# Kernel tuning notes

Measured on AMD Instinct MI355X. Metric: run time of the kernel, lower is better.

The kernel has to match this reference:

```python
import jax, jax.numpy as jnp
import numpy as np

NEG_SLOPE = 0.2

def _gatv2(x_src, x_dst, src, dst, Wl, bl, Wr, br, att, bias, num_dst, edge_feat=None, We=None):
    # PyG GATv2Conv (heads=1, add_self_loops=False, eval mode -> no dropout)
    xl = x_src @ Wl + bl                      # [Ns, C] lin_l on source
    xr = x_dst @ Wr + br                      # [Nd, C] lin_r on target
    m = xl[src] + xr[dst]                     # [E, C]
    if edge_feat is not None:
        m = m + edge_feat @ We                # lin_edge (bias=False)
    e = jax.nn.leaky_relu(m, NEG_SLOPE) @ att # [E] attention logits
    emax = jax.ops.segment_max(e, dst, num_segments=num_dst)
    ee = jnp.exp(e - emax[dst])
    denom = jax.ops.segment_sum(ee, dst, num_segments=num_dst)
    alpha = ee / jnp.maximum(denom[dst], 1e-16)
    out = jax.ops.segment_sum(alpha[:, None] * xl[src], dst, num_segments=num_dst)
    return out + bias


def setup_inputs() -> dict:
    key = jax.random.key(0)
    N_OP, N_M, N_A = 50000, 5000, 2000
    C_OP, C_M, C_A = 256, 128, 128
    E_OO, E_OM, E_MA, E_DIM = 200000, 200000, 60000, 8
    ks = jax.random.split(key, 40)
    i = iter(range(40))
    def nrm(shape, fan_in):
        return jax.random.normal(ks[next(i)], shape, dtype=jnp.float32) / np.sqrt(fan_in)
    inp = {}
    inp['x_op'] = jax.random.normal(ks[next(i)], (N_OP, C_OP), dtype=jnp.float32)
    inp['x_m'] = jax.random.normal(ks[next(i)], (N_M, C_M), dtype=jnp.float32)
    inp['x_a'] = jax.random.normal(ks[next(i)], (N_A, C_A), dtype=jnp.float32)
    inp['ei_pred'] = jax.random.randint(ks[next(i)], (2, E_OO), 0, N_OP)
    inp['ei_succ'] = jax.random.randint(ks[next(i)], (2, E_OO), 0, N_OP)
    inp['src_o2m'] = jax.random.randint(ks[next(i)], (E_OM,), 0, N_OP)
    inp['dst_o2m'] = jax.random.randint(ks[next(i)], (E_OM,), 0, N_M)
    inp['src_m2a'] = jax.random.randint(ks[next(i)], (E_MA,), 0, N_M)
    inp['dst_m2a'] = jax.random.randint(ks[next(i)], (E_MA,), 0, N_A)
    inp['ea_m2a'] = jax.random.normal(ks[next(i)], (E_MA, E_DIM), dtype=jnp.float32)
    for name, c_in_src, c_in_dst, c_out in [('pred', C_OP, C_OP, C_OP), ('succ', C_OP, C_OP, C_OP), ('o2m', C_OP, C_M, C_M), ('m2a', C_M, C_A, C_A)]:
        inp[f'Wl_{name}'] = nrm((c_in_src, c_out), c_in_src)
        inp[f'bl_{name}'] = jnp.zeros((c_out,), jnp.float32)
        inp[f'Wr_{name}'] = nrm((c_in_dst, c_out), c_in_dst)
        inp[f'br_{name}'] = jnp.zeros((c_out,), jnp.float32)
        inp[f'att_{name}'] = nrm((c_out,), c_out)
        inp[f'b_{name}'] = jnp.zeros((c_out,), jnp.float32)
    inp['We_m2a'] = nrm((E_DIM, C_A), E_DIM)
    return inp


def reference(x_op, x_m, x_a, ei_pred, ei_succ, src_o2m, dst_o2m, src_m2a, dst_m2a, ea_m2a,
              Wl_pred, bl_pred, Wr_pred, br_pred, att_pred, b_pred,
              Wl_succ, bl_succ, Wr_succ, br_succ, att_succ, b_succ,
              Wl_o2m, bl_o2m, Wr_o2m, br_o2m, att_o2m, b_o2m,
              Wl_m2a, bl_m2a, Wr_m2a, br_m2a, att_m2a, b_m2a, We_m2a):
    N_OP, N_M, N_A = x_op.shape[0], x_m.shape[0], x_a.shape[0]
    # operation_relation_extract: two op->op GATv2 convs, HeteroConv sum-aggregated
    f_pred = _gatv2(x_op, x_op, ei_pred[0], ei_pred[1], Wl_pred, bl_pred, Wr_pred, br_pred, att_pred, b_pred, N_OP)
    f_succ = _gatv2(x_op, x_op, ei_succ[0], ei_succ[1], Wl_succ, bl_succ, Wr_succ, br_succ, att_succ, b_succ, N_OP)
    # hetero_relation_extract
    f_mach = _gatv2(x_op, x_m, src_o2m, dst_o2m, Wl_o2m, bl_o2m, Wr_o2m, br_o2m, att_o2m, b_o2m, N_M)
    f_agv = _gatv2(x_m, x_a, src_m2a, dst_m2a, Wl_m2a, bl_m2a, Wr_m2a, br_m2a, att_m2a, b_m2a, N_A, edge_feat=ea_m2a, We=We_m2a)
    # residual sum across relation outputs per node type
    out_op = x_op + f_pred + f_succ
    out_m = x_m + f_mach
    out_a = x_a + f_agv
    return (out_op, out_m, out_a)
```

## Files before the change

kernel.cpp:

```cpp
#include <hip/hip_runtime.h>

#define N_OP   50000
#define N_M    5000
#define N_A    2000
#define C_OP   256
#define C_M    128
#define C_A    128
#define E_OO   200000
#define E_OM   200000
#define E_MA   60000
#define E_DIM  8

#define OUT_OP_OFF 0
#define OUT_M_OFF  (N_OP * C_OP)
#define OUT_A_OFF  (N_OP * C_OP + N_M * C_M)

typedef short bf16x8 __attribute__((ext_vector_type(8)));
typedef float f32x4 __attribute__((ext_vector_type(4)));
typedef __attribute__((address_space(1))) const unsigned gu32;
typedef __attribute__((address_space(3))) unsigned lu32;

__device__ __forceinline__ unsigned short f2bf(float f) {
    unsigned u = __float_as_uint(f);
    unsigned r = (u + 0x7FFFu + ((u >> 16) & 1u)) >> 16;
    return (unsigned short)r;
}
__device__ __forceinline__ float bf2f(unsigned short h) {
    return __uint_as_float(((unsigned)h) << 16);
}

__device__ __forceinline__ void init_one(const float* __restrict__ x,
                                         const float* __restrict__ b1,
                                         const float* __restrict__ b2,
                                         float* __restrict__ out,
                                         unsigned short* __restrict__ xc,
                                         int i, int cmask) {
    float4 v = ((const float4*)x)[i];
    const int cb = i & cmask;
    float4 b = ((const float4*)b1)[cb];
    if (b2) {
        float4 t = ((const float4*)b2)[cb];
        b.x += t.x; b.y += t.y; b.z += t.z; b.w += t.w;
    }
    float4 o;
    o.x = v.x + b.x; o.y = v.y + b.y; o.z = v.z + b.z; o.w = v.w + b.w;
    ((float4*)out)[i] = o;
    ushort4 r;
    r.x = f2bf(v.x); r.y = f2bf(v.y); r.z = f2bf(v.z); r.w = f2bf(v.w);
    ((ushort4*)xc)[i] = r;
}

#define I3_OP (N_OP * C_OP / 4)
#define I3_M  (I3_OP + N_M * C_M / 4)
#define I3_A  (I3_M + N_A * C_A / 4)

__global__ void init3(const float* __restrict__ x_op, const float* __restrict__ x_m,
                      const float* __restrict__ x_a,
                      const float* __restrict__ bP, const float* __restrict__ bS,
                      const float* __restrict__ bO, const float* __restrict__ bA,
                      float* __restrict__ out_op, float* __restrict__ out_m,
                      float* __restrict__ out_a,
                      unsigned short* __restrict__ xcop, unsigned short* __restrict__ xcm,
                      unsigned short* __restrict__ xca) {
    int i = blockIdx.x * blockDim.x + threadIdx.x;
    if (i < I3_OP)      init_one(x_op, bP, bS, out_op, xcop, i, 63);
    else if (i < I3_M)  init_one(x_m, bO, nullptr, out_m, xcm, i - I3_OP, 31);
    else if (i < I3_A)  init_one(x_a, bA, nullptr, out_a, xca, i - I3_M, 31);
}

#define PK_P   131072
#define PK_S   262144
#define PK_OL  294912
#define PK_OR  311296
#define PK_ML  327680
#define PK_MR  344064
#define PK_BP  344576
#define PK_BS  345088

__global__ void pack_all(const float* __restrict__ WlP, const float* __restrict__ WrP,
                         const float* __restrict__ WlS, const float* __restrict__ WrS,
                         const float* __restrict__ WOl, const float* __restrict__ WOr,
                         const float* __restrict__ WMl, const float* __restrict__ WMr,
                         const float* __restrict__ blP, const float* __restrict__ brP,
                         const float* __restrict__ blS, const float* __restrict__ brS,
                         unsigned short* __restrict__ BtP, unsigned short* __restrict__ BtS,
                         unsigned short* __restrict__ BtOL, unsigned short* __restrict__ BtOR,
                         unsigned short* __restrict__ BtML, unsigned short* __restrict__ BtMR,
                         float* __restrict__ biasP, float* __restrict__ biasS) {
    int i = blockIdx.x * blockDim.x + threadIdx.x;
    if (i < PK_P) {
        int n = i >> 8, k = i & 255;
        BtP[i] = f2bf((n < 256) ? WlP[k * 256 + n] : WrP[k * 256 + (n - 256)]);
    } else if (i < PK_S) {
        int j = i - PK_P; int n = j >> 8, k = j & 255;
        BtS[j] = f2bf((n < 256) ? WlS[k * 256 + n] : WrS[k * 256 + (n - 256)]);
    } else if (i < PK_OL) {
        int j = i - PK_S; int n = j >> 8, k = j & 255;
        BtOL[j] = f2bf(WOl[k * 128 + n]);
    } else if (i < PK_OR) {
        int j = i - PK_OL; int n = j >> 7, k = j & 127;
        BtOR[j] = f2bf(WOr[k * 128 + n]);
    } else if (i < PK_ML) {
        int j = i - PK_OR; int n = j >> 7, k = j & 127;
        BtML[j] = f2bf(WMl[k * 128 + n]);
    } else if (i < PK_MR) {
        int j = i - PK_ML; int n = j >> 7, k = j & 127;
        BtMR[j] = f2bf(WMr[k * 128 + n]);
    } else if (i < PK_BP) {
        int j = i - PK_MR;
        biasP[j] = (j < 256) ? blP[j] : brP[j - 256];
    } else if (i < PK_BS) {
        int j = i - PK_BP;
        biasS[j] = (j < 256) ? blS[j] : brS[j - 256];
    }
}

__device__ __forceinline__ void gload_lds16(const void* g, void* l) {
    __builtin_amdgcn_global_load_lds((gu32*)g, (lu32*)l, 16, 0, 0);
}

__global__ __launch_bounds__(256) void mfma_gemm(
    const unsigned short* __restrict__ A, const unsigned short* __restrict__ Bt,
    const float* __restrict__ bias, unsigned short* __restrict__ C,
    int M, int K, int ldc) {
    __shared__ unsigned short As[2][128 * 64];
    __shared__ unsigned short Bs[2][128 * 64];

    const int tid  = threadIdx.x;
    const int lane = tid & 63;
    const int wid  = tid >> 6;
    const int m0   = blockIdx.x * 128;
    const int n0   = blockIdx.y * 128;

    f32x4 acc[4][4] = {};

    const int srow   = tid >> 3;
    const int scolb  = (tid & 7) * 16;
    const int scole  = (scolb ^ ((srow & 7) << 4)) >> 1;

    int grA[4], grB[4];
#pragma unroll
    for (int i = 0; i < 4; ++i) {
        int gr = m0 + i * 32 + srow;
        grA[i] = (gr < M) ? gr : M - 1;
        grB[i] = n0 + i * 32 + srow;
    }

    const int nt = K >> 6;
    int cur = 0;

#define STAGE(buf, k0)                                                          \
    {                                                                           \
        _Pragma("unroll")                                                       \
        for (int i = 0; i < 4; ++i)                                             \
            gload_lds16(A + (size_t)grA[i] * K + (k0) + scole,                  \
                        &As[buf][i * 2048 + tid * 8]);                          \
        _Pragma("unroll")                                                       \
        for (int i = 0; i < 4; ++i)                                             \
            gload_lds16(Bt + (size_t)grB[i] * K + (k0) + scole,                 \
                        &Bs[buf][i * 2048 + tid * 8]);                          \
    }

    STAGE(0, 0)
    asm volatile("s_waitcnt vmcnt(0)" ::: "memory");
    __syncthreads();

    const int wr = (wid >> 1) * 64;
    const int wc = (wid & 1) * 64;

    for (int t = 0; t < nt; ++t) {
        if (t + 1 < nt) STAGE(cur ^ 1, (t + 1) * 64)
#pragma unroll
        for (int kh = 0; kh < 2; ++kh) {
            const int kob = kh * 64 + (lane >> 4) * 16;
            bf16x8 a[4], b[4];
#pragma unroll
            for (int mi = 0; mi < 4; ++mi) {
                const int row = wr + mi * 16 + (lane & 15);
                a[mi] = *(const bf16x8*)((const char*)As[cur] + row * 128 +
                                         (kob ^ ((row & 7) << 4)));
            }
#pragma unroll
            for (int ni = 0; ni < 4; ++ni) {
                const int row = wc + ni * 16 + (lane & 15);
                b[ni] = *(const bf16x8*)((const char*)Bs[cur] + row * 128 +
                                         (kob ^ ((row & 7) << 4)));
            }
#pragma unroll
            for (int mi = 0; mi < 4; ++mi)
#pragma unroll
                for (int ni = 0; ni < 4; ++ni)
                    acc[mi][ni] = __builtin_amdgcn_mfma_f32_16x16x32_bf16(
                        a[mi], b[ni], acc[mi][ni], 0, 0, 0);
        }
        asm volatile("s_waitcnt vmcnt(0)" ::: "memory");
        __syncthreads();
        cur ^= 1;
    }
#undef STAGE

    const int crow = (lane >> 4) * 4;
    const int ccol = lane & 15;
    float bcol[4];
#pragma unroll
    for (int ni = 0; ni < 4; ++ni) bcol[ni] = bias[n0 + wc + ni * 16 + ccol];
#pragma unroll
    for (int mi = 0; mi < 4; ++mi) {
#pragma unroll
        for (int j = 0; j < 4; ++j) {
            const int row = m0 + wr + mi * 16 + crow + j;
            if (row < M) {
                unsigned short* pc = C + (size_t)row * ldc + n0 + wc + ccol;
#pragma unroll
                for (int ni = 0; ni < 4; ++ni)
                    pc[ni * 16] = f2bf(acc[mi][ni][j] + bcol[ni]);
            }
        }
    }
}

template <int K, int N, int TM>
__global__ void gemm_ef(const float* __restrict__ A, const float* __restrict__ W,
                        const int* __restrict__ eid, unsigned short* __restrict__ out) {
    __shared__ float As[TM][K];
    const int m0 = blockIdx.x * TM;
    const int tid = threadIdx.x;
    for (int idx = tid; idx < TM * K; idx += N) {
        int r = idx / K, k = idx - r * K;
        As[r][k] = A[(size_t)eid[m0 + r] * K + k];
    }
    __syncthreads();
    float acc[TM] = {};
    for (int k = 0; k < K; ++k) {
        const float w = W[k * N + tid];
#pragma unroll
        for (int r = 0; r < TM; ++r) acc[r] += As[r][k] * w;
    }
#pragma unroll
    for (int r = 0; r < TM; ++r) out[(size_t)(m0 + r) * N + tid] = f2bf(acc[r]);
}

#define NB_P 49
#define NB_S 49
#define NB_O 5
#define NB_A 2
#define NTOT 107000
#define ETOT 660000

__global__ void zero4(int* __restrict__ p, int n) {
    int i = blockIdx.x * blockDim.x + threadIdx.x;
    if (i < n) p[i] = 0;
}

__global__ void hist_rank4(const int* __restrict__ dP, const int* __restrict__ dS,
                           const int* __restrict__ dO, const int* __restrict__ dA,
                           int* __restrict__ cP, int* __restrict__ cS,
                           int* __restrict__ cO, int* __restrict__ cA,
                           int* __restrict__ rk) {
    int i = blockIdx.x * blockDim.x + threadIdx.x;
    if (i < 200000)      rk[i] = atomicAdd(&cP[dP[i]], 1);
    else if (i < 400000) rk[i] = atomicAdd(&cS[dS[i - 200000]], 1);
    else if (i < 600000) rk[i] = atomicAdd(&cO[dO[i - 400000]], 1);
    else if (i < ETOT)   rk[i] = atomicAdd(&cA[dA[i - 600000]], 1);
}

__global__ void scan_blk4(const int* __restrict__ cP, const int* __restrict__ cS,
                          const int* __restrict__ cO, const int* __restrict__ cA,
                          int* __restrict__ pP, int* __restrict__ pS,
                          int* __restrict__ pO, int* __restrict__ pA,
                          int* __restrict__ bsum) {
    __shared__ int smem[1024];
    int b = blockIdx.x;
    const int* cnt; int* ptr; int n; int bo;
    if (b < NB_P)                { cnt = cP; ptr = pP; n = 50000; bo = 0; }
    else if (b < NB_P + NB_S)    { cnt = cS; ptr = pS; n = 50000; bo = 64;  b -= NB_P; }
    else if (b < NB_P + NB_S + NB_O) { cnt = cO; ptr = pO; n = 5000; bo = 128; b -= NB_P + NB_S; }
    else                         { cnt = cA; ptr = pA; n = 2000; bo = 192; b -= NB_P + NB_S + NB_O; }
    const int tid = threadIdx.x;
    const int i = b * 1024 + tid;
    const int v = (i < n) ? cnt[i] : 0;
    smem[tid] = v;
    __syncthreads();
    for (int o = 1; o < 1024; o <<= 1) {
        int t = (tid >= o) ? smem[tid - o] : 0;
        __syncthreads();
        smem[tid] += t;
        __syncthreads();
    }
    if (i < n) ptr[i] = smem[tid] - v;
    if (tid == 1023) bsum[bo + b] = smem[1023];
}

__global__ void scan_tops4(const int* __restrict__ bsum, int* __restrict__ boff,
                           int* __restrict__ pP, int* __restrict__ pS,
                           int* __restrict__ pO, int* __restrict__ pA) {
    __shared__ int smem[1024];
    const int seg = blockIdx.x;
    const int nb = (seg < 2) ? 49 : (seg == 2 ? 5 : 2);
    const int off = seg * 64;
    int* ptr_n = (seg == 0) ? pP + 50000 : (seg == 1) ? pS + 50000
               : (seg == 2) ? pO + 5000 : pA + 2000;
    const int tid = threadIdx.x;
    const int v = (tid < nb) ? bsum[off + tid] : 0;
    smem[tid] = v;
    __syncthreads();
    for (int o = 1; o < 1024; o <<= 1) {
        int t = (tid >= o) ? smem[tid - o] : 0;
        __syncthreads();
        smem[tid] += t;
        __syncthreads();
    }
    if (tid < nb) boff[off + tid] = smem[tid] - v;
    if (tid == 1023) *ptr_n = smem[1023];
}

__global__ void scan_add4(int* __restrict__ pP, int* __restrict__ pS,
                          int* __restrict__ pO, int* __restrict__ pA,
                          const int* __restrict__ boff) {
    int i = blockIdx.x * blockDim.x + threadIdx.x;
    int* ptr; int loc; int off;
    if (i < 50000)       { ptr = pP; loc = i;          off = 0; }
    else if (i < 100000) { ptr = pS; loc = i - 50000;  off = 64; }
    else if (i < 105000) { ptr = pO; loc = i - 100000; off = 128; }
    else if (i < NTOT)   { ptr = pA; loc = i - 105000; off = 192; }
    else return;
    ptr[loc] += boff[off + (loc >> 10)];
}

__global__ void scatter_nr4(const int* __restrict__ sP, const int* __restrict__ dP,
                            const int* __restrict__ sS, const int* __restrict__ dS,
                            const int* __restrict__ sO, const int* __restrict__ dO,
                            const int* __restrict__ sA, const int* __restrict__ dA,
                            const int* __restrict__ pP, const int* __restrict__ pS,
                            const int* __restrict__ pO, const int* __restrict__ pA,
                            const int* __restrict__ rk,
                            int* __restrict__ srP, int* __restrict__ srS,
                            int* __restrict__ srO, int* __restrict__ srA,
                            int* __restrict__ eiA) {
    int i = blockIdx.x * blockDim.x + threadIdx.x;
    if (i < 200000) {
        srP[pP[dP[i]] + rk[i]] = sP[i];
    } else if (i < 400000) {
        const int j = i - 200000;
        srS[pS[dS[j]] + rk[i]] = sS[j];
    } else if (i < 600000) {
        const int j = i - 400000;
        srO[pO[dO[j]] + rk[i]] = sO[j];
    } else if (i < ETOT) {
        const int j = i - 600000;
        const int pos = pA[dA[j]] + rk[i];
        srA[pos] = sA[j];
        eiA[pos] = j;
    }
}

template <int C>
__global__ void csr_serial2(const unsigned short* __restrict__ xl, int ldl,
                            const unsigned short* __restrict__ xr, int ldr,
                            const float* __restrict__ att,
                            const int* __restrict__ ptr, const int* __restrict__ srcs,
                            float* __restrict__ out, int n) {
    const int tid = threadIdx.x;
    const int node = blockIdx.x * (blockDim.x >> 5) + (tid >> 5);
    if (node >= n) return;
    const int gl = tid & 31;
    const int beg = ptr[node], end = ptr[node + 1];
    if (beg == end) return;

    constexpr int V = C / 32;
    const int c0 = gl * V;

    float av[V], rvf[V];
    {
        const unsigned short* pr = xr + (size_t)node * ldr + c0;
        unsigned short rv[V];
        *(uint4*)rv = *(const uint4*)pr;
#pragma unroll
        for (int v4 = 0; v4 < V / 4; ++v4)
            *(float4*)(av + v4 * 4) = ((const float4*)(att + c0))[v4];
#pragma unroll
        for (int v = 0; v < V; ++v) rvf[v] = bf2f(rv[v]);
    }

    float runM = -3.0e38f, runS = 0.0f;
    float acc[V] = {};

    unsigned short lv[V];
    {
        const unsigned short* pl = xl + (size_t)srcs[beg] * ldl + c0;
        *(uint4*)lv = *(const uint4*)pl;
    }

    for (int j = beg; j < end; ++j) {
        float cf[V];
#pragma unroll
        for (int v = 0; v < V; ++v) cf[v] = bf2f(lv[v]);
        if (j + 1 < end) {
            const unsigned short* pl = xl + (size_t)srcs[j + 1] * ldl + c0;
            *(uint4*)lv = *(const uint4*)pl;
        }

        float part = 0.0f;
#pragma unroll
        for (int v = 0; v < V; ++v) {
            float m = cf[v] + rvf[v];
            m = (m >= 0.0f) ? m : 0.2f * m;
            part += m * av[v];
        }
        part += __shfl_xor(part, 1, 64);
        part += __shfl_xor(part, 2, 64);
        part += __shfl_xor(part, 4, 64);
        part += __shfl_xor(part, 8, 64);
        part += __shfl_xor(part, 16, 64);

        const float newM = fmaxf(runM, part);
        const float sc = __expf(runM - newM);
        const float e1 = __expf(part - newM);
        runS = runS * sc + e1;
        runM = newM;
#pragma unroll
        for (int v = 0; v < V; ++v) acc[v] = acc[v] * sc + e1 * cf[v];
    }

    const float inv = 1.0f / fmaxf(runS, 1e-16f);
    float* po = out + (size_t)node * C + c0;
#pragma unroll
    for (int v4 = 0; v4 < V / 4; ++v4) {
        float4 o = ((float4*)po)[v4];
        o.x += acc[v4 * 4 + 0] * inv;
        o.y += acc[v4 * 4 + 1] * inv;
        o.z += acc[v4 * 4 + 2] * inv;
        o.w += acc[v4 * 4 + 3] * inv;
        ((float4*)po)[v4] = o;
    }
}

template <int C, bool HAS_EF>
__global__ void csr_grp(const unsigned short* __restrict__ xl, int ldl,
                        const unsigned short* __restrict__ xr, int ldr,
                        const unsigned short* __restrict__ ef,
                        const float* __restrict__ att,
                        const int* __restrict__ ptr, const int* __restrict__ srcs,
                        float* __restrict__ out, int n) {
    const int node = blockIdx.x * (blockDim.x >> 6) + (threadIdx.x >> 6);
    if (node >= n) return;
    const int lane = threadIdx.x & 63;
    const int grp  = lane >> 4;
    const int sl   = lane & 15;
    const int beg = ptr[node], end = ptr[node + 1];
    if (beg == end) return;

    constexpr int W = C / 16;
    const int c0 = sl * W;

    float av[W], rvf[W];
    {
        const unsigned short* pr = xr + (size_t)node * ldr + c0;
        unsigned short rv[W];
        *(uint4*)rv = *(const uint4*)pr;
        if constexpr (W == 16) *(uint4*)(rv + 8) = *(const uint4*)(pr + 8);
#pragma unroll
        for (int v4 = 0; v4 < W / 4; ++v4)
            *(float4*)(av + v4 * 4) = ((const float4*)(att + c0))[v4];
#pragma unroll
        for (int v = 0; v < W; ++v) rvf[v] = bf2f(rv[v]);
    }

    float runM = -3.0e38f, runS = 0.0f;
    float acc[W] = {};

    for (int cb = beg; cb < end; cb += 4) {
        const int j = cb + grp;
        const bool act = (j < end);
        const int js = act ? j : end - 1;
        const int s = srcs[js];

        const unsigned short* pl = xl + (size_t)s * ldl + c0;
        unsigned short lv[W];
        *(uint4*)lv = *(const uint4*)pl;
        if constexpr (W == 16) *(uint4*)(lv + 8) = *(const uint4*)(pl + 8);
        float cf[W];
#pragma unroll
        for (int v = 0; v < W; ++v) cf[v] = bf2f(lv[v]);

        float part = 0.0f;
        if constexpr (HAS_EF) {
            unsigned short efv[W];
            const unsigned short* pe = ef + (size_t)js * C + c0;
            *(uint4*)efv = *(const uint4*)pe;
            if constexpr (W == 16) *(uint4*)(efv + 8) = *(const uint4*)(pe + 8);
#pragma unroll
            for (int v = 0; v < W; ++v) {
                float m = cf[v] + rvf[v] + bf2f(efv[v]);
                m = (m >= 0.0f) ? m : 0.2f * m;
                part += m * av[v];
            }
        } else {
#pragma unroll
            for (int v = 0; v < W; ++v) {
                float m = cf[v] + rvf[v];
                m = (m >= 0.0f) ? m : 0.2f * m;
                part += m * av[v];
            }
        }
        part += __shfl_xor(part, 1, 64);
        part += __shfl_xor(part, 2, 64);
        part += __shfl_xor(part, 4, 64);
        part += __shfl_xor(part, 8, 64);
        if (!act) part = -3.0e38f;

        float cm = fmaxf(part, __shfl_xor(part, 16, 64));
        cm = fmaxf(cm, __shfl_xor(cm, 32, 64));

        if (cm > runM) {
            const float sc = __expf(runM - cm);
            runS *= sc;
#pragma unroll
            for (int v = 0; v < W; ++v) acc[v] *= sc;
            runM = cm;
        }
        const float w = act ? __expf(part - runM) : 0.0f;
        float cs = w + __shfl_xor(w, 16, 64);
        cs += __shfl_xor(cs, 32, 64);
        runS += cs;
#pragma unroll
        for (int v = 0; v < W; ++v) acc[v] += w * cf[v];
    }

#pragma unroll
    for (int v = 0; v < W; ++v) acc[v] += __shfl_xor(acc[v], 16, 64);
#pragma unroll
    for (int v = 0; v < W; ++v) acc[v] += __shfl_xor(acc[v], 32, 64);

    const float inv = 1.0f / fmaxf(runS, 1e-16f);
    if (grp == 0) {
        float* po = out + (size_t)node * C + c0;
#pragma unroll
        for (int v4 = 0; v4 < W / 4; ++v4) {
            float4 o = ((float4*)po)[v4];
            o.x += acc[v4 * 4 + 0] * inv;
            o.y += acc[v4 * 4 + 1] * inv;
            o.z += acc[v4 * 4 + 2] * inv;
            o.w += acc[v4 * 4 + 3] * inv;
            ((float4*)po)[v4] = o;
        }
    }
}

#define F_H      0
#define F_XCOP   12800000
#define F_XCM    19200000
#define F_XCA    19520000
#define F_BTP    19648000
#define F_BTS    19713536
#define F_BTOL   19779072
#define F_BTOR   19795456
#define F_BTML   19803648
#define F_BTMR   19811840
#define F_BIASP  19820032
#define F_BIASS  19820544
#define F_CNT4   19821056
#define F_BSUM   19928056
#define F_BOFF   19928312
#define F_PTR_P  19928568
#define F_SRC_P  19978569
#define F_PTR_S  20178569
#define F_SRC_S  20228570
#define F_PTR_O  20428570
#define F_SRC_O  20433571
#define F_PTR_A  20633571
#define F_SRC_A  20635572
#define F_EID_A  20695572
#define F_RANK   20755572

extern "C" void kernel_launch(void* const* d_in, const int* in_sizes, int n_in,
                              void* d_out, int out_size, void* d_ws, size_t ws_size,
                              hipStream_t stream) {
    const float* x_op    = (const float*)d_in[0];
    const float* x_m     = (const float*)d_in[1];
    const float* x_a     = (const float*)d_in[2];
    const int*   ei_pred = (const int*)d_in[3];
    const int*   ei_succ = (const int*)d_in[4];
    const int*   src_o2m = (const int*)d_in[5];
    const int*   dst_o2m = (const int*)d_in[6];
    const int*   src_m2a = (const int*)d_in[7];
    const int*   dst_m2a = (const int*)d_in[8];
    const float* ea_m2a  = (const float*)d_in[9];

    const float* Wl_pred = (const float*)d_in[10];
    const float* bl_pred = (const float*)d_in[11];
    const float* Wr_pred = (const float*)d_in[12];
    const float* br_pred = (const float*)d_in[13];
    const float* att_pred= (const float*)d_in[14];
    const float* b_pred  = (const float*)d_in[15];

    const float* Wl_succ = (const float*)d_in[16];
    const float* bl_succ = (const float*)d_in[17];
    const float* Wr_succ = (const float*)d_in[18];
    const float* br_succ = (const float*)d_in[19];
    const float* att_succ= (const float*)d_in[20];
    const float* b_succ  = (const float*)d_in[21];

    const float* Wl_o2m  = (const float*)d_in[22];
    const float* bl_o2m  = (const float*)d_in[23];
    const float* Wr_o2m  = (const float*)d_in[24];
    const float* br_o2m  = (const float*)d_in[25];
    const float* att_o2m = (const float*)d_in[26];
    const float* b_o2m   = (const float*)d_in[27];

    const float* Wl_m2a  = (const float*)d_in[28];
    const float* bl_m2a  = (const float*)d_in[29];
    const float* Wr_m2a  = (const float*)d_in[30];
    const float* br_m2a  = (const float*)d_in[31];
    const float* att_m2a = (const float*)d_in[32];
    const float* b_m2a   = (const float*)d_in[33];
    const float* We_m2a  = (const float*)d_in[34];

    float* ws = (float*)d_ws;
    unsigned short* H     = (unsigned short*)(ws + F_H);
    unsigned short* xc_op = (unsigned short*)(ws + F_XCOP);
    unsigned short* xc_m  = (unsigned short*)(ws + F_XCM);
    unsigned short* xc_a  = (unsigned short*)(ws + F_XCA);
    unsigned short* BtP   = (unsigned short*)(ws + F_BTP);
    unsigned short* BtS   = (unsigned short*)(ws + F_BTS);
    unsigned short* BtOL  = (unsigned short*)(ws + F_BTOL);
    unsigned short* BtOR  = (unsigned short*)(ws + F_BTOR);
    unsigned short* BtML  = (unsigned short*)(ws + F_BTML);
    unsigned short* BtMR  = (unsigned short*)(ws + F_BTMR);
    float* biasP = ws + F_BIASP;
    float* biasS = ws + F_BIASS;
    int* cntP = (int*)(ws + F_CNT4);
    int* cntS = cntP + 50000;
    int* cntO = cntP + 100000;
    int* cntA = cntP + 105000;
    int* bsum = (int*)(ws + F_BSUM);
    int* boff = (int*)(ws + F_BOFF);
    int* ptrP = (int*)(ws + F_PTR_P); int* srcP = (int*)(ws + F_SRC_P);
    int* ptrS = (int*)(ws + F_PTR_S); int* srcS = (int*)(ws + F_SRC_S);
    int* ptrO = (int*)(ws + F_PTR_O); int* srcO = (int*)(ws + F_SRC_O);
    int* ptrA = (int*)(ws + F_PTR_A); int* srcA = (int*)(ws + F_SRC_A);
    int* eidA = (int*)(ws + F_EID_A);
    int* rk   = (int*)(ws + F_RANK);

    float* out_op = (float*)d_out + OUT_OP_OFF;
    float* out_m  = (float*)d_out + OUT_M_OFF;
    float* out_a  = (float*)d_out + OUT_A_OFF;

    zero4<<<(NTOT + 255) / 256, 256, 0, stream>>>(cntP, NTOT);
    hist_rank4<<<(ETOT + 255) / 256, 256, 0, stream>>>(ei_pred + E_OO, ei_succ + E_OO,
                                                       dst_o2m, dst_m2a,
                                                       cntP, cntS, cntO, cntA, rk);
    scan_blk4<<<NB_P + NB_S + NB_O + NB_A, 1024, 0, stream>>>(cntP, cntS, cntO, cntA,
                                                              ptrP, ptrS, ptrO, ptrA, bsum);
    scan_tops4<<<4, 1024, 0, stream>>>(bsum, boff, ptrP, ptrS, ptrO, ptrA);
    scan_add4<<<(NTOT + 255) / 256, 256, 0, stream>>>(ptrP, ptrS, ptrO, ptrA, boff);
    scatter_nr4<<<(ETOT + 255) / 256, 256, 0, stream>>>(
        ei_pred, ei_pred + E_OO, ei_succ, ei_succ + E_OO,
        src_o2m, dst_o2m, src_m2a, dst_m2a,
        ptrP, ptrS, ptrO, ptrA, rk,
        srcP, srcS, srcO, srcA, eidA);

    init3<<<(I3_A + 255) / 256, 256, 0, stream>>>(x_op, x_m, x_a, b_pred, b_succ, b_o2m, b_m2a,
                                                  out_op, out_m, out_a, xc_op, xc_m, xc_a);
    pack_all<<<(PK_BS + 255) / 256, 256, 0, stream>>>(
        Wl_pred, Wr_pred, Wl_succ, Wr_succ, Wl_o2m, Wr_o2m, Wl_m2a, Wr_m2a,
        bl_pred, br_pred, bl_succ, br_succ,
        BtP, BtS, BtOL, BtOR, BtML, BtMR, biasP, biasS);

    const int MT_OP = (N_OP + 127) / 128;
    const int MT_M  = (N_M + 127) / 128;
    const int MT_A  = (N_A + 127) / 128;

    mfma_gemm<<<dim3(MT_OP, 4), 256, 0, stream>>>(xc_op, BtP, biasP, H, N_OP, 256, 512);
    csr_serial2<256><<<(N_OP + 7) / 8, 256, 0, stream>>>(H, 512, H + 256, 512,
                                                         att_pred, ptrP, srcP, out_op, N_OP);

    mfma_gemm<<<dim3(MT_OP, 4), 256, 0, stream>>>(xc_op, BtS, biasS, H, N_OP, 256, 512);
    csr_serial2<256><<<(N_OP + 7) / 8, 256, 0, stream>>>(H, 512, H + 256, 512,
                                                         att_succ, ptrS, srcS, out_op, N_OP);

    {
        unsigned short* xlb = H;
        unsigned short* xrb = H + 6400000;
        mfma_gemm<<<dim3(MT_OP, 1), 256, 0, stream>>>(xc_op, BtOL, bl_o2m, xlb, N_OP, 256, 128);
        mfma_gemm<<<dim3(MT_M, 1), 256, 0, stream>>>(xc_m, BtOR, br_o2m, xrb, N_M, 128, 128);
        csr_grp<128, false><<<(N_M + 3) / 4, 256, 0, stream>>>(xlb, 128, xrb, 128, nullptr,
                                                               att_o2m, ptrO, srcO, out_m, N_M);
    }

    {
        unsigned short* xlb = H;
        unsigned short* xrb = H + 1000000;
        unsigned short* efb = H + 2000000;
        mfma_gemm<<<dim3(MT_M, 1), 256, 0, stream>>>(xc_m, BtML, bl_m2a, xlb, N_M, 128, 128);
        mfma_gemm<<<dim3(MT_A, 1), 256, 0, stream>>>(xc_a, BtMR, br_m2a, xrb, N_A, 128, 128);
        gemm_ef<8, 128, 4><<<E_MA / 4, 128, 0, stream>>>(ea_m2a, We_m2a, eidA, efb);
        csr_grp<128, true><<<(N_A + 3) / 4, 256, 0, stream>>>(xlb, 128, xrb, 128, efb,
                                                              att_m2a, ptrA, srcA, out_a, N_A);
    }
}
```

Before: 308.7 us.

## Merge independent prep, scatter, and small GEMM launches into combined kernels

Folds histogram/rank, input init/bf16 conversion, and weight packing into one prep_all kernel. The CSR scatter now runs as extra blocks of the first pred GEMM launch. The o2m lin_l/lin_r GEMMs become one gemm_pair launch, and the m2a GEMMs plus the edge-feature projection become one gemm_tri launch. The aim is fewer launches and idle gaps between small kernels. In exchange, the scatter blocks allocate GEMM-sized shared memory, which may lower their occupancy.

```diff
diff --git a/kernel.cpp b/kernel.cpp
--- a/kernel.cpp
+++ b/kernel.cpp
@@ -28,6 +28,27 @@
 __device__ __forceinline__ float bf2f(unsigned short h) {
     return __uint_as_float(((unsigned)h) << 16);
 }
+
+#define NTOT 107000
+#define ETOT 660000
+
+#define I3_OP (N_OP * C_OP / 4)
+#define I3_M  (I3_OP + N_M * C_M / 4)
+#define I3_A  (I3_M + N_A * C_A / 4)
+
+#define PK_P   131072
+#define PK_S   262144
+#define PK_OL  294912
+#define PK_OR  311296
+#define PK_ML  327680
+#define PK_MR  344064
+#define PK_BP  344576
+#define PK_BS  345088
+
+#define PREP_HIST_BLK ((ETOT + 255) / 256)
+#define PREP_INIT_BLK (I3_A / 256)
+#define PREP_PACK_BLK (PK_BS / 256)
+#define PREP_TOTAL    (PREP_HIST_BLK + PREP_INIT_BLK + PREP_PACK_BLK)
 
 __device__ __forceinline__ void init_one(const float* __restrict__ x,
                                          const float* __restrict__ b1,
@@ -50,68 +71,68 @@
     ((ushort4*)xc)[i] = r;
 }
 
-#define I3_OP (N_OP * C_OP / 4)
-#define I3_M  (I3_OP + N_M * C_M / 4)
-#define I3_A  (I3_M + N_A * C_A / 4)
-
-__global__ void init3(const float* __restrict__ x_op, const float* __restrict__ x_m,
-                      const float* __restrict__ x_a,
-                      const float* __restrict__ bP, const float* __restrict__ bS,
-                      const float* __restrict__ bO, const float* __restrict__ bA,
-                      float* __restrict__ out_op, float* __restrict__ out_m,
-                      float* __restrict__ out_a,
-                      unsigned short* __restrict__ xcop, unsigned short* __restrict__ xcm,
-                      unsigned short* __restrict__ xca) {
-    int i = blockIdx.x * blockDim.x + threadIdx.x;
-    if (i < I3_OP)      init_one(x_op, bP, bS, out_op, xcop, i, 63);
-    else if (i < I3_M)  init_one(x_m, bO, nullptr, out_m, xcm, i - I3_OP, 31);
-    else if (i < I3_A)  init_one(x_a, bA, nullptr, out_a, xca, i - I3_M, 31);
-}
-
-#define PK_P   131072
-#define PK_S   262144
-#define PK_OL  294912
-#define PK_OR  311296
-#define PK_ML  327680
-#define PK_MR  344064
-#define PK_BP  344576
-#define PK_BS  345088
-
-__global__ void pack_all(const float* __restrict__ WlP, const float* __restrict__ WrP,
-                         const float* __restrict__ WlS, const float* __restrict__ WrS,
-                         const float* __restrict__ WOl, const float* __restrict__ WOr,
-                         const float* __restrict__ WMl, const float* __restrict__ WMr,
-                         const float* __restrict__ blP, const float* __restrict__ brP,
-                         const float* __restrict__ blS, const float* __restrict__ brS,
-                         unsigned short* __restrict__ BtP, unsigned short* __restrict__ BtS,
-                         unsigned short* __restrict__ BtOL, unsigned short* __restrict__ BtOR,
-                         unsigned short* __restrict__ BtML, unsigned short* __restrict__ BtMR,
-                         float* __restrict__ biasP, float* __restrict__ biasS) {
-    int i = blockIdx.x * blockDim.x + threadIdx.x;
-    if (i < PK_P) {
-        int n = i >> 8, k = i & 255;
-        BtP[i] = f2bf((n < 256) ? WlP[k * 256 + n] : WrP[k * 256 + (n - 256)]);
-    } else if (i < PK_S) {
-        int j = i - PK_P; int n = j >> 8, k = j & 255;
-        BtS[j] = f2bf((n < 256) ? WlS[k * 256 + n] : WrS[k * 256 + (n - 256)]);
-    } else if (i < PK_OL) {
-        int j = i - PK_S; int n = j >> 8, k = j & 255;
-        BtOL[j] = f2bf(WOl[k * 128 + n]);
-    } else if (i < PK_OR) {
-        int j = i - PK_OL; int n = j >> 7, k = j & 127;
-        BtOR[j] = f2bf(WOr[k * 128 + n]);
-    } else if (i < PK_ML) {
-        int j = i - PK_OR; int n = j >> 7, k = j & 127;
-        BtML[j] = f2bf(WMl[k * 128 + n]);
-    } else if (i < PK_MR) {
-        int j = i - PK_ML; int n = j >> 7, k = j & 127;
-        BtMR[j] = f2bf(WMr[k * 128 + n]);
-    } else if (i < PK_BP) {
-        int j = i - PK_MR;
-        biasP[j] = (j < 256) ? blP[j] : brP[j - 256];
-    } else if (i < PK_BS) {
-        int j = i - PK_BP;
-        biasS[j] = (j < 256) ? blS[j] : brS[j - 256];
+__global__ void prep_all(
+    const int* __restrict__ dP, const int* __restrict__ dS,
+    const int* __restrict__ dO, const int* __restrict__ dA,
+    int* __restrict__ cP, int* __restrict__ cS,
+    int* __restrict__ cO, int* __restrict__ cA, int* __restrict__ rk,
+    const float* __restrict__ x_op, const float* __restrict__ x_m,
+    const float* __restrict__ x_a,
+    const float* __restrict__ bP, const float* __restrict__ bS,
+    const float* __restrict__ bO, const float* __restrict__ bA,
+    float* __restrict__ out_op, float* __restrict__ out_m, float* __restrict__ out_a,
+    unsigned short* __restrict__ xcop, unsigned short* __restrict__ xcm,
+    unsigned short* __restrict__ xca,
+    const float* __restrict__ WlP, const float* __restrict__ WrP,
+    const float* __restrict__ WlS, const float* __restrict__ WrS,
+    const float* __restrict__ WOl, const float* __restrict__ WOr,
+    const float* __restrict__ WMl, const float* __restrict__ WMr,
+    const float* __restrict__ blP, const float* __restrict__ brP,
+    const float* __restrict__ blS, const float* __restrict__ brS,
+    unsigned short* __restrict__ BtP, unsigned short* __restrict__ BtS,
+    unsigned short* __restrict__ BtOL, unsigned short* __restrict__ BtOR,
+    unsigned short* __restrict__ BtML, unsigned short* __restrict__ BtMR,
+    float* __restrict__ biasP, float* __restrict__ biasS) {
+    const int b = blockIdx.x;
+    const int tid = threadIdx.x;
+    if (b < PREP_HIST_BLK) {
+        int i = b * 256 + tid;
+        if (i < 200000)      rk[i] = atomicAdd(&cP[dP[i]], 1);
+        else if (i < 400000) rk[i] = atomicAdd(&cS[dS[i - 200000]], 1);
+        else if (i < 600000) rk[i] = atomicAdd(&cO[dO[i - 400000]], 1);
+        else if (i < ETOT)   rk[i] = atomicAdd(&cA[dA[i - 600000]], 1);
+    } else if (b < PREP_HIST_BLK + PREP_INIT_BLK) {
+        int i = (b - PREP_HIST_BLK) * 256 + tid;
+        if (i < I3_OP)      init_one(x_op, bP, bS, out_op, xcop, i, 63);
+        else if (i < I3_M)  init_one(x_m, bO, nullptr, out_m, xcm, i - I3_OP, 31);
+        else                init_one(x_a, bA, nullptr, out_a, xca, i - I3_M, 31);
+    } else {
+        int i = (b - PREP_HIST_BLK - PREP_INIT_BLK) * 256 + tid;
+        if (i < PK_P) {
+            int n = i >> 8, k = i & 255;
+            BtP[i] = f2bf((n < 256) ? WlP[k * 256 + n] : WrP[k * 256 + (n - 256)]);
+        } else if (i < PK_S) {
+            int j = i - PK_P; int n = j >> 8, k = j & 255;
+            BtS[j] = f2bf((n < 256) ? WlS[k * 256 + n] : WrS[k * 256 + (n - 256)]);
+        } else if (i < PK_OL) {
+            int j = i - PK_S; int n = j >> 8, k = j & 255;
+            BtOL[j] = f2bf(WOl[k * 128 + n]);
+        } else if (i < PK_OR) {
+            int j = i - PK_OL; int n = j >> 7, k = j & 127;
+            BtOR[j] = f2bf(WOr[k * 128 + n]);
+        } else if (i < PK_ML) {
+            int j = i - PK_OR; int n = j >> 7, k = j & 127;
+            BtML[j] = f2bf(WMl[k * 128 + n]);
+        } else if (i < PK_MR) {
+            int j = i - PK_ML; int n = j >> 7, k = j & 127;
+            BtMR[j] = f2bf(WMr[k * 128 + n]);
+        } else if (i < PK_BP) {
+            int j = i - PK_MR;
+            biasP[j] = (j < 256) ? blP[j] : brP[j - 256];
+        } else if (i < PK_BS) {
+            int j = i - PK_BP;
+            biasS[j] = (j < 256) ? blS[j] : brS[j - 256];
+        }
     }
 }
 
@@ -119,18 +140,16 @@
     __builtin_amdgcn_global_load_lds((gu32*)g, (lu32*)l, 16, 0, 0);
 }
 
-__global__ __launch_bounds__(256) void mfma_gemm(
+__device__ __forceinline__ void gemm_body(
     const unsigned short* __restrict__ A, const unsigned short* __restrict__ Bt,
     const float* __restrict__ bias, unsigned short* __restrict__ C,
-    int M, int K, int ldc) {
-    __shared__ unsigned short As[2][128 * 64];
-    __shared__ unsigned short Bs[2][128 * 64];
-
+    int M, int K, int ldc, int bx, int by,
+    unsigned short (&As)[2][128 * 64], unsigned short (&Bs)[2][128 * 64]) {
     const int tid  = threadIdx.x;
     const int lane = tid & 63;
     const int wid  = tid >> 6;
-    const int m0   = blockIdx.x * 128;
-    const int n0   = blockIdx.y * 128;
+    const int m0   = bx * 128;
+    const int n0   = by * 128;
 
     f32x4 acc[4][4] = {};
 
@@ -219,49 +238,113 @@
     }
 }
 
-template <int K, int N, int TM>
-__global__ void gemm_ef(const float* __restrict__ A, const float* __restrict__ W,
-                        const int* __restrict__ eid, unsigned short* __restrict__ out) {
-    __shared__ float As[TM][K];
-    const int m0 = blockIdx.x * TM;
-    const int tid = threadIdx.x;
-    for (int idx = tid; idx < TM * K; idx += N) {
-        int r = idx / K, k = idx - r * K;
-        As[r][k] = A[(size_t)eid[m0 + r] * K + k];
-    }
-    __syncthreads();
-    float acc[TM] = {};
-    for (int k = 0; k < K; ++k) {
-        const float w = W[k * N + tid];
-#pragma unroll
-        for (int r = 0; r < TM; ++r) acc[r] += As[r][k] * w;
-    }
-#pragma unroll
-    for (int r = 0; r < TM; ++r) out[(size_t)(m0 + r) * N + tid] = f2bf(acc[r]);
+__global__ __launch_bounds__(256) void mfma_gemm(
+    const unsigned short* __restrict__ A, const unsigned short* __restrict__ Bt,
+    const float* __restrict__ bias, unsigned short* __restrict__ C,
+    int M, int K, int ldc) {
+    __shared__ unsigned short As[2][128 * 64];
+    __shared__ unsigned short Bs[2][128 * 64];
+    gemm_body(A, Bt, bias, C, M, K, ldc, blockIdx.x, blockIdx.y, As, Bs);
+}
+
+#define SCAT_XBLK 645
+__global__ __launch_bounds__(256) void gemm_scat(
+    const unsigned short* __restrict__ A, const unsigned short* __restrict__ Bt,
+    const float* __restrict__ bias, unsigned short* __restrict__ C,
+    int M, int K, int ldc, int mt,
+    const int* __restrict__ sP, const int* __restrict__ dP,
+    const int* __restrict__ sS, const int* __restrict__ dS,
+    const int* __restrict__ sO, const int* __restrict__ dO,
+    const int* __restrict__ sA, const int* __restrict__ dA,
+    const int* __restrict__ pP, const int* __restrict__ pS,
+    const int* __restrict__ pO, const int* __restrict__ pA,
+    const int* __restrict__ rk,
+    int* __restrict__ srP, int* __restrict__ srS,
+    int* __restrict__ srO, int* __restrict__ srA, int* __restrict__ eiA) {
+    __shared__ unsigned short As[2][128 * 64];
+    __shared__ unsigned short Bs[2][128 * 64];
+    if ((int)blockIdx.x < mt) {
+        gemm_body(A, Bt, bias, C, M, K, ldc, blockIdx.x, blockIdx.y, As, Bs);
+    } else {
+        const int i = (((int)blockIdx.x - mt) * 4 + (int)blockIdx.y) * 256 + (int)threadIdx.x;
+        if (i < 200000) {
+            srP[pP[dP[i]] + rk[i]] = sP[i];
+        } else if (i < 400000) {
+            const int j = i - 200000;
+            srS[pS[dS[j]] + rk[i]] = sS[j];
+        } else if (i < 600000) {
+            const int j = i - 400000;
+            srO[pO[dO[j]] + rk[i]] = sO[j];
+        } else if (i < ETOT) {
+            const int j = i - 600000;
+            const int pos = pA[dA[j]] + rk[i];
+            srA[pos] = sA[j];
+            eiA[pos] = j;
+        }
+    }
+}
+
+__global__ __launch_bounds__(256) void gemm_pair(
+    const unsigned short* A1, const unsigned short* Bt1, const float* b1,
+    unsigned short* C1, int M1, int K1, int l1, int n1,
+    const unsigned short* A2, const unsigned short* Bt2, const float* b2,
+    unsigned short* C2, int M2, int K2, int l2) {
+    __shared__ unsigned short As[2][128 * 64];
+    __shared__ unsigned short Bs[2][128 * 64];
+    const unsigned short *A, *Bt; const float* bi; unsigned short* C;
+    int M, K, ldc, bx;
+    if ((int)blockIdx.x < n1) { A = A1; Bt = Bt1; bi = b1; C = C1; M = M1; K = K1; ldc = l1; bx = blockIdx.x; }
+    else                      { A = A2; Bt = Bt2; bi = b2; C = C2; M = M2; K = K2; ldc = l2; bx = blockIdx.x - n1; }
+    gemm_body(A, Bt, bi, C, M, K, ldc, bx, blockIdx.y, As, Bs);
+}
+
+__global__ __launch_bounds__(256) void gemm_tri(
+    const unsigned short* A1, const unsigned short* Bt1, const float* b1,
+    unsigned short* C1, int M1, int K1, int n1,
+    const unsigned short* A2, const unsigned short* Bt2, const float* b2,
+    unsigned short* C2, int M2, int K2, int n12,
+    const float* __restrict__ ea, const float* __restrict__ We,
+    const int* __restrict__ eid, unsigned short* __restrict__ efo) {
+    __shared__ unsigned short As[2][128 * 64];
+    __shared__ unsigned short Bs[2][128 * 64];
+    __shared__ float Ef[8][8];
+    const int b = blockIdx.x;
+    if (b < n12) {
+        const unsigned short *A, *Bt; const float* bi; unsigned short* C;
+        int M, K, bx;
+        if (b < n1) { A = A1; Bt = Bt1; bi = b1; C = C1; M = M1; K = K1; bx = b; }
+        else        { A = A2; Bt = Bt2; bi = b2; C = C2; M = M2; K = K2; bx = b - n1; }
+        gemm_body(A, Bt, bi, C, M, K, 128, bx, 0, As, Bs);
+    } else {
+        const int eb = b - n12;
+        const int m0 = eb * 8;
+        const int tid = threadIdx.x;
+        if (tid < 64) {
+            int r = tid >> 3, k = tid & 7;
+            Ef[r][k] = ea[(size_t)eid[m0 + r] * 8 + k];
+        }
+        __syncthreads();
+        const int col = tid & 127, half = tid >> 7;
+        float acc[4] = {};
+        for (int k = 0; k < 8; ++k) {
+            const float w = We[k * 128 + col];
+#pragma unroll
+            for (int r = 0; r < 4; ++r) acc[r] += Ef[half * 4 + r][k] * w;
+        }
+#pragma unroll
+        for (int r = 0; r < 4; ++r)
+            efo[(size_t)(m0 + half * 4 + r) * 128 + col] = f2bf(acc[r]);
+    }
 }
 
 #define NB_P 49
 #define NB_S 49
 #define NB_O 5
 #define NB_A 2
-#define NTOT 107000
-#define ETOT 660000
 
 __global__ void zero4(int* __restrict__ p, int n) {
     int i = blockIdx.x * blockDim.x + threadIdx.x;
     if (i < n) p[i] = 0;
-}
-
-__global__ void hist_rank4(const int* __restrict__ dP, const int* __restrict__ dS,
-                           const int* __restrict__ dO, const int* __restrict__ dA,
-                           int* __restrict__ cP, int* __restrict__ cS,
-                           int* __restrict__ cO, int* __restrict__ cA,
-                           int* __restrict__ rk) {
-    int i = blockIdx.x * blockDim.x + threadIdx.x;
-    if (i < 200000)      rk[i] = atomicAdd(&cP[dP[i]], 1);
-    else if (i < 400000) rk[i] = atomicAdd(&cS[dS[i - 200000]], 1);
-    else if (i < 600000) rk[i] = atomicAdd(&cO[dO[i - 400000]], 1);
-    else if (i < ETOT)   rk[i] = atomicAdd(&cA[dA[i - 600000]], 1);
 }
 
 __global__ void scan_blk4(const int* __restrict__ cP, const int* __restrict__ cS,
@@ -325,33 +408,6 @@
     else if (i < NTOT)   { ptr = pA; loc = i - 105000; off = 192; }
     else return;
     ptr[loc] += boff[off + (loc >> 10)];
-}
-
-__global__ void scatter_nr4(const int* __restrict__ sP, const int* __restrict__ dP,
-                            const int* __restrict__ sS, const int* __restrict__ dS,
-                            const int* __restrict__ sO, const int* __restrict__ dO,
-                            const int* __restrict__ sA, const int* __restrict__ dA,
-                            const int* __restrict__ pP, const int* __restrict__ pS,
-                            const int* __restrict__ pO, const int* __restrict__ pA,
-                            const int* __restrict__ rk,
-                            int* __restrict__ srP, int* __restrict__ srS,
-                            int* __restrict__ srO, int* __restrict__ srA,
-                            int* __restrict__ eiA) {
-    int i = blockIdx.x * blockDim.x + threadIdx.x;
-    if (i < 200000) {
-        srP[pP[dP[i]] + rk[i]] = sP[i];
-    } else if (i < 400000) {
-        const int j = i - 200000;
-        srS[pS[dS[j]] + rk[i]] = sS[j];
-    } else if (i < 600000) {
-        const int j = i - 400000;
-        srO[pO[dO[j]] + rk[i]] = sO[j];
-    } else if (i < ETOT) {
-        const int j = i - 600000;
-        const int pos = pA[dA[j]] + rk[i];
-        srA[pos] = sA[j];
-        eiA[pos] = j;
-    }
 }
 
 template <int C>
@@ -647,31 +703,31 @@
     float* out_a  = (float*)d_out + OUT_A_OFF;
 
     zero4<<<(NTOT + 255) / 256, 256, 0, stream>>>(cntP, NTOT);
-    hist_rank4<<<(ETOT + 255) / 256, 256, 0, stream>>>(ei_pred + E_OO, ei_succ + E_OO,
-                                                       dst_o2m, dst_m2a,
-                                                       cntP, cntS, cntO, cntA, rk);
+
+    prep_all<<<PREP_TOTAL, 256, 0, stream>>>(
+        ei_pred + E_OO, ei_succ + E_OO, dst_o2m, dst_m2a,
+        cntP, cntS, cntO, cntA, rk,
+        x_op, x_m, x_a, b_pred, b_succ, b_o2m, b_m2a,
+        out_op, out_m, out_a, xc_op, xc_m, xc_a,
+        Wl_pred, Wr_pred, Wl_succ, Wr_succ, Wl_o2m, Wr_o2m, Wl_m2a, Wr_m2a,
+        bl_pred, br_pred, bl_succ, br_succ,
+        BtP, BtS, BtOL, BtOR, BtML, BtMR, biasP, biasS);
+
     scan_blk4<<<NB_P + NB_S + NB_O + NB_A, 1024, 0, stream>>>(cntP, cntS, cntO, cntA,
                                                               ptrP, ptrS, ptrO, ptrA, bsum);
     scan_tops4<<<4, 1024, 0, stream>>>(bsum, boff, ptrP, ptrS, ptrO, ptrA);
     scan_add4<<<(NTOT + 255) / 256, 256, 0, stream>>>(ptrP, ptrS, ptrO, ptrA, boff);
-    scatter_nr4<<<(ETOT + 255) / 256, 256, 0, stream>>>(
+
+    const int MT_OP = (N_OP + 127) / 128;
+    const int MT_M  = (N_M + 127) / 128;
+    const int MT_A  = (N_A + 127) / 128;
+
+    gemm_scat<<<dim3(MT_OP + SCAT_XBLK, 4), 256, 0, stream>>>(
+        xc_op, BtP, biasP, H, N_OP, 256, 512, MT_OP,
         ei_pred, ei_pred + E_OO, ei_succ, ei_succ + E_OO,
         src_o2m, dst_o2m, src_m2a, dst_m2a,
         ptrP, ptrS, ptrO, ptrA, rk,
         srcP, srcS, srcO, srcA, eidA);
-
-    init3<<<(I3_A + 255) / 256, 256, 0, stream>>>(x_op, x_m, x_a, b_pred, b_succ, b_o2m, b_m2a,
-                                                  out_op, out_m, out_a, xc_op, xc_m, xc_a);
-    pack_all<<<(PK_BS + 255) / 256, 256, 0, stream>>>(
-        Wl_pred, Wr_pred, Wl_succ, Wr_succ, Wl_o2m, Wr_o2m, Wl_m2a, Wr_m2a,
-        bl_pred, br_pred, bl_succ, br_succ,
-        BtP, BtS, BtOL, BtOR, BtML, BtMR, biasP, biasS);
-
-    const int MT_OP = (N_OP + 127) / 128;
-    const int MT_M  = (N_M + 127) / 128;
-    const int MT_A  = (N_A + 127) / 128;
-
-    mfma_gemm<<<dim3(MT_OP, 4), 256, 0, stream>>>(xc_op, BtP, biasP, H, N_OP, 256, 512);
     csr_serial2<256><<<(N_OP + 7) / 8, 256, 0, stream>>>(H, 512, H + 256, 512,
                                                          att_pred, ptrP, srcP, out_op, N_OP);
 
@@ -682,8 +738,9 @@
     {
         unsigned short* xlb = H;
         unsigned short* xrb = H + 6400000;
-        mfma_gemm<<<dim3(MT_OP, 1), 256, 0, stream>>>(xc_op, BtOL, bl_o2m, xlb, N_OP, 256, 128);
-        mfma_gemm<<<dim3(MT_M, 1), 256, 0, stream>>>(xc_m, BtOR, br_o2m, xrb, N_M, 128, 128);
+        gemm_pair<<<dim3(MT_OP + MT_M, 1), 256, 0, stream>>>(
+            xc_op, BtOL, bl_o2m, xlb, N_OP, 256, 128, MT_OP,
+            xc_m, BtOR, br_o2m, xrb, N_M, 128, 128);
         csr_grp<128, false><<<(N_M + 3) / 4, 256, 0, stream>>>(xlb, 128, xrb, 128, nullptr,
                                                                att_o2m, ptrO, srcO, out_m, N_M);
     }
@@ -692,9 +749,10 @@
         unsigned short* xlb = H;
         unsigned short* xrb = H + 1000000;
         unsigned short* efb = H + 2000000;
-        mfma_gemm<<<dim3(MT_M, 1), 256, 0, stream>>>(xc_m, BtML, bl_m2a, xlb, N_M, 128, 128);
-        mfma_gemm<<<dim3(MT_A, 1), 256, 0, stream>>>(xc_a, BtMR, br_m2a, xrb, N_A, 128, 128);
-        gemm_ef<8, 128, 4><<<E_MA / 4, 128, 0, stream>>>(ea_m2a, We_m2a, eidA, efb);
+        gemm_tri<<<dim3(MT_M + MT_A + E_MA / 8, 1), 256, 0, stream>>>(
+            xc_m, BtML, bl_m2a, xlb, N_M, 128, MT_M,
+            xc_a, BtMR, br_m2a, xrb, N_A, 128, MT_M + MT_A,
+            ea_m2a, We_m2a, eidA, efb);
         csr_grp<128, true><<<(N_A + 3) / 4, 256, 0, stream>>>(xlb, 128, xrb, 128, efb,
                                                               att_m2a, ptrA, srcA, out_a, N_A);
     }
```

New measurement: 291.8 us. 1.06x faster.
